# Optimization experiments

Measured on AMD Instinct MI355X. Metric: run time of the kernel, lower is better.

The kernel has to match this reference:

```python
import jax, jax.numpy as jnp
import numpy as np

B, S, C, H, FF = 2, 1500, 1024, 16, 4096
D = C // H  # head_dim = 64
EPS = 1e-5


def _ln(x, g, b):
    # LayerNorm over channel dim (axis=1) for (B, C, S) tensors
    mu = jnp.mean(x, axis=1, keepdims=True)
    var = jnp.mean(jnp.square(x - mu), axis=1, keepdims=True)
    return (x - mu) * jax.lax.rsqrt(var + EPS) * g[None, :, None] + b[None, :, None]


def setup_inputs() -> dict:
    key = jax.random.key(0)
    ks = jax.random.split(key, 24)
    w = lambda k, shp: (jax.random.normal(k, shp, dtype=jnp.float32) * 0.02)
    return {
        "hidden_states": jax.random.normal(ks[0], (B, C, 1, S), dtype=jnp.float32),
        "attention_mask": jnp.ones((B, S), dtype=jnp.float32),
        "position_bias": jax.random.normal(ks[1], (B, H, S, S), dtype=jnp.float32),
        "Wq": w(ks[2], (C, C)), "bq": jnp.zeros((C,), jnp.float32),
        "Wk": w(ks[3], (C, C)), "bk": jnp.zeros((C,), jnp.float32),
        "Wv": w(ks[4], (C, C)), "bv": jnp.zeros((C,), jnp.float32),
        "Wo": w(ks[5], (C, C)), "bo": jnp.zeros((C,), jnp.float32),
        "Wg": w(ks[6], (8, D)), "bg": jnp.zeros((8,), jnp.float32),
        "gru_const": jnp.ones((1, 1, H, 1), jnp.float32),
        "ln1_g": jnp.ones((C,), jnp.float32), "ln1_b": jnp.zeros((C,), jnp.float32),
        "W1": w(ks[7], (FF, C)), "b1": jnp.zeros((FF,), jnp.float32),
        "W2": w(ks[8], (C, FF)), "b2": jnp.zeros((C,), jnp.float32),
        "ln2_g": jnp.ones((C,), jnp.float32), "ln2_b": jnp.zeros((C,), jnp.float32),
    }


def reference(hidden_states, attention_mask, position_bias,
              Wq, bq, Wk, bk, Wv, bv, Wo, bo, Wg, bg, gru_const,
              ln1_g, ln1_b, W1, b1, W2, b2, ln2_g, ln2_b):
    x = hidden_states[:, :, 0, :]  # (B, C, S)

    # --- GRU-style relative-position gate ---
    xh = x.reshape(B, H, D, S)  # (B, H, D, S)
    # conv2d with (8, D, 1, 1) kernel on (B, D, H, S) == per-head linear D->8
    g8 = jnp.einsum('od,bhds->bohs', Wg, xh) + bg[None, :, None, None]  # (B, 8, H, S)
    gate_a = jax.nn.sigmoid(jnp.sum(g8[:, :4], axis=1, keepdims=True))  # (B, 1, H, S)
    gate_b = jax.nn.sigmoid(jnp.sum(g8[:, 4:], axis=1, keepdims=True))  # (B, 1, H, S)
    gate = gate_a * (gate_b * gru_const - 1.0) + 2.0  # (B, 1, H, S)
    qk_mask = gate[:, 0, :, :, None] * position_bias  # (B, H, Sq, Sk)

    # --- self-attention ---
    q = (jnp.einsum('oc,bcs->bos', Wq, x) + bq[None, :, None]).reshape(B, H, D, S)
    k = (jnp.einsum('oc,bcs->bos', Wk, x) + bk[None, :, None]).reshape(B, H, D, S)
    v = (jnp.einsum('oc,bcs->bos', Wv, x) + bv[None, :, None]).reshape(B, H, D, S)
    scale = 1.0 / jnp.sqrt(jnp.float32(D))
    kpm = (1.0 - attention_mask) * -10000.0  # (B, S)
    scores = jnp.einsum('bhdq,bhdk->bhqk', q, k) * scale + qk_mask + kpm[:, None, None, :]
    probs = jax.nn.softmax(scores, axis=-1)
    ctx = jnp.einsum('bhqk,bhdk->bhdq', probs, v).reshape(B, C, S)
    attn_out = jnp.einsum('oc,bcs->bos', Wo, ctx) + bo[None, :, None]

    h = _ln(x + attn_out, ln1_g, ln1_b)

    # --- FFN ---
    f = jax.nn.gelu(jnp.einsum('fc,bcs->bfs', W1, h) + b1[None, :, None], approximate=False)
    f = jnp.einsum('cf,bfs->bcs', W2, f) + b2[None, :, None]

    out = _ln(h + f, ln2_g, ln2_b)
    return out[:, :, None, :]  # (B, C, 1, S)
```

## Files before the change

kernel.cpp:

```cpp
#include <hip/hip_runtime.h>
#include <cstddef>
#include <cstdint>

#define Bn 2
#define Sn 1500
#define SPn 1536
#define Cn 1024
#define Hn 16
#define FFn 4096

typedef __attribute__((ext_vector_type(8))) short bf16x8;
typedef __attribute__((ext_vector_type(4))) float f32x4;
typedef unsigned short u16;
typedef unsigned int u32;

__device__ __forceinline__ u16 f2bu(float f) {
  unsigned u = __float_as_uint(f);
  return (u16)((u + 0x7fffu + ((u >> 16) & 1u)) >> 16);
}

__device__ __forceinline__ void gl_lds16(const u16* g, u16* l) {
  __builtin_amdgcn_global_load_lds(
      (__attribute__((address_space(1))) void*)(uintptr_t)g,
      (__attribute__((address_space(3))) void*)(u32)(uintptr_t)l,
      16, 0, 0);
}

__global__ __launch_bounds__(256) void k_pre(
    const float* __restrict__ x,
    const float* __restrict__ Wq, const float* __restrict__ Wk,
    const float* __restrict__ Wv, const float* __restrict__ Wo,
    const float* __restrict__ W1, const float* __restrict__ W2,
    const float* __restrict__ bq, const float* __restrict__ bk,
    const float* __restrict__ bv,
    const float* __restrict__ Wg, const float* __restrict__ bg,
    const float* __restrict__ gc,
    float* __restrict__ xT, u16* __restrict__ xTb,
    u16* __restrict__ wqkvb, u16* __restrict__ wob,
    u16* __restrict__ w1b, u16* __restrict__ w2b, float* __restrict__ bqkv,
    float* __restrict__ gate)
{
  const int bid = blockIdx.x;
  if (bid < 3072) {
    __shared__ float t[32][33];
    const int c0 = (bid & 31) * 32, s0 = ((bid >> 5) % 48) * 32, b = bid / 1536;
    const int tx = threadIdx.x & 31, ty = threadIdx.x >> 5;
#pragma unroll
    for (int i = 0; i < 32; i += 8) {
      int c = c0 + ty + i, s = s0 + tx;
      t[ty + i][tx] = (s < Sn) ? x[((size_t)b * Cn + c) * Sn + s] : 0.f;
    }
    __syncthreads();
#pragma unroll
    for (int i = 0; i < 32; i += 8) {
      int s = s0 + ty + i, c = c0 + tx;
      float v = t[tx][ty + i];
      size_t o = ((size_t)b * SPn + s) * Cn + c;
      xT[o] = v;
      xTb[o] = f2bu(v);
    }
    return;
  }
  if (bid < 15363) {
    int i = (bid - 3072) * 256 + threadIdx.x;
    const float* src;
    u16* dst;
    int j;
    if (i < 786432) {
      src = (i < 262144) ? Wq : ((i < 524288) ? Wk : Wv);
      j = i & 262143;
      dst = wqkvb + (size_t)i * 4;
    } else if (i < 1048576) {
      src = Wo; j = i - 786432; dst = wob + (size_t)j * 4;
    } else if (i < 2097152) {
      src = W1; j = i - 1048576; dst = w1b + (size_t)j * 4;
    } else if (i < 3145728) {
      src = W2; j = i - 2097152; dst = w2b + (size_t)j * 4;
    } else {
      int k = i - 3145728;
      const float* bsrc = (k < 256) ? bq : ((k < 512) ? bk : bv);
      float4 v = *(const float4*)(bsrc + (k & 255) * 4);
      *(float4*)(bqkv + k * 4) = v;
      return;
    }
    float4 v = *(const float4*)(src + (size_t)j * 4);
    ushort4 o;
    o.x = f2bu(v.x); o.y = f2bu(v.y); o.z = f2bu(v.z); o.w = f2bu(v.w);
    *(ushort4*)dst = o;
    return;
  }
  {
    const int gid = bid - 15363;
    const int b = gid / 96, h = (gid / 6) & 15;
    const int s = (gid % 6) * 256 + threadIdx.x;
    const bool vld = s < Sn;
    const float* xp = x + ((size_t)b * Cn + h * 64) * Sn + (vld ? s : 0);
    float dot[8];
#pragma unroll
    for (int o = 0; o < 8; o++) dot[o] = 0.f;
    for (int d = 0; d < 64; d++) {
      float v = xp[(size_t)d * Sn];
#pragma unroll
      for (int o = 0; o < 8; o++) dot[o] += Wg[o * 64 + d] * v;
    }
    float sa = dot[0] + dot[1] + dot[2] + dot[3] + bg[0] + bg[1] + bg[2] + bg[3];
    float sb = dot[4] + dot[5] + dot[6] + dot[7] + bg[4] + bg[5] + bg[6] + bg[7];
    float ga = 1.f / (1.f + __expf(-sa));
    float gb = 1.f / (1.f + __expf(-sb));
    float gv = ga * (gb * gc[h] - 1.f) + 2.f;
    gate[((size_t)b * Hn + h) * SPn + s] = vld ? gv : 0.f;
  }
}

__global__ __launch_bounds__(256) void k_transpose_out(
    const float* __restrict__ oT, float* __restrict__ o)
{
  __shared__ float t[32][33];
  const int b = blockIdx.z, c0 = blockIdx.x * 32, s0 = blockIdx.y * 32;
  const int tx = threadIdx.x & 31, ty = threadIdx.x >> 5;
#pragma unroll
  for (int i = 0; i < 32; i += 8) {
    int s = s0 + ty + i, c = c0 + tx;
    t[ty + i][tx] = oT[((size_t)b * SPn + s) * Cn + c];
  }
  __syncthreads();
#pragma unroll
  for (int i = 0; i < 32; i += 8) {
    int c = c0 + ty + i, s = s0 + tx;
    if (s < Sn) o[((size_t)b * Cn + c) * Sn + s] = t[tx][ty + i];
  }
}

template <int EPI, int SPLIT, int TM>
__global__ __launch_bounds__(256) void k_gemm(
    const u16* __restrict__ A, const u16* __restrict__ X,
    const float* __restrict__ bias, void* __restrict__ out, void* __restrict__ out2,
    u16* __restrict__ vT, int M, int Kst, int Ktot)
{
  constexpr int NI = TM / 32;
  const int zz = blockIdx.z;
  const int b = zz / SPLIT, half = zz % SPLIT;
  const int Kc = Ktot / SPLIT;
  const int m0 = blockIdx.x * TM;
  const int s0 = blockIdx.y * 128;
  const int tid = threadIdx.x;
  const int lane = tid & 63;
  const int wid = tid >> 6;
  const int wm = (wid >> 1) * (TM / 2);
  const int wn = (wid & 1) * 64;
  const int l15 = lane & 15;
  const int g4 = lane >> 4;

  __shared__ __align__(16) u16 lA[TM][64];
  __shared__ __align__(16) u16 lX[128][64];

  f32x4 acc[NI][4];
  f32x4 zr; zr[0] = 0.f; zr[1] = 0.f; zr[2] = 0.f; zr[3] = 0.f;
#pragma unroll
  for (int i = 0; i < NI; i++)
#pragma unroll
    for (int j = 0; j < 4; j++) acc[i][j] = zr;

  const int rlo = lane >> 3;
  const int cg = (lane & 7) ^ rlo;
  const int kbeg = half * Kc;
  const u16* gA = A + (size_t)(m0 + wid * (TM / 4) + rlo) * Kst + cg * 8 + kbeg;
  const u16* gX = X + ((size_t)b * SPn + s0 + wid * 32 + rlo) * Kst + cg * 8 + kbeg;
  u16* lAp = &lA[0][0] + wid * (TM / 4) * 64;
  u16* lXp = &lX[0][0] + wid * 2048;
  const size_t rstep8 = (size_t)8 * Kst;

  for (int kt = 0; kt < Kc; kt += 64) {
    __syncthreads();
#pragma unroll
    for (int j = 0; j < TM / 32; j++)
      gl_lds16(gA + j * rstep8 + kt, lAp + j * 512);
#pragma unroll
    for (int j = 0; j < 4; j++)
      gl_lds16(gX + j * rstep8 + kt, lXp + j * 512);
    __syncthreads();
#pragma unroll
    for (int ks = 0; ks < 2; ks++) {
      bf16x8 af[NI], bfr[4];
#pragma unroll
      for (int i = 0; i < NI; i++) {
        int ra = wm + i * 16 + l15;
        af[i] = *(const bf16x8*)&lA[ra][((ks * 4 + g4) ^ (ra & 7)) * 8];
      }
#pragma unroll
      for (int j = 0; j < 4; j++) {
        int rb = wn + j * 16 + l15;
        bfr[j] = *(const bf16x8*)&lX[rb][((ks * 4 + g4) ^ (rb & 7)) * 8];
      }
#pragma unroll
      for (int i = 0; i < NI; i++)
#pragma unroll
        for (int j = 0; j < 4; j++)
          acc[i][j] = __builtin_amdgcn_mfma_f32_16x16x32_bf16(af[i], bfr[j], acc[i][j], 0, 0, 0);
    }
  }

  const float hsc = (half == 0) ? 1.f : 0.f;
  void* outp = (half == 0) ? out : out2;
#pragma unroll
  for (int i = 0; i < NI; i++) {
    int o = m0 + wm + i * 16 + g4 * 4;
    float4 bs = *(const float4*)(bias + o);
#pragma unroll
    for (int j = 0; j < 4; j++) {
      int s = s0 + wn + j * 16 + l15;
      size_t oidx = ((size_t)b * SPn + s) * M + o;
      f32x4 v = acc[i][j];
      float x0 = v[0] + bs.x * hsc, x1 = v[1] + bs.y * hsc;
      float x2 = v[2] + bs.z * hsc, x3 = v[3] + bs.w * hsc;
      if (EPI == 0) {
        float4 st; st.x = x0; st.y = x1; st.z = x2; st.w = x3;
        *(float4*)((float*)outp + oidx) = st;
      } else if (EPI == 1) {
        x0 = 0.5f * x0 * (1.f + erff(x0 * 0.70710678118654752f));
        x1 = 0.5f * x1 * (1.f + erff(x1 * 0.70710678118654752f));
        x2 = 0.5f * x2 * (1.f + erff(x2 * 0.70710678118654752f));
        x3 = 0.5f * x3 * (1.f + erff(x3 * 0.70710678118654752f));
        ushort4 st;
        st.x = f2bu(x0); st.y = f2bu(x1); st.z = f2bu(x2); st.w = f2bu(x3);
        *(ushort4*)((u16*)outp + oidx) = st;
      } else {
        ushort4 st;
        st.x = f2bu(x0); st.y = f2bu(x1); st.z = f2bu(x2); st.w = f2bu(x3);
        *(ushort4*)((u16*)outp + oidx) = st;
        if (EPI == 2 && o >= 2048) {
          int oo = o - 2048;
          int h = oo >> 6, d = oo & 63;
          u16* vp = vT + ((size_t)(b * Hn + h) * 64 + d) * SPn + s;
          vp[0] = st.x;
          vp[SPn] = st.y;
          vp[2 * SPn] = st.z;
          vp[3 * SPn] = st.w;
        }
      }
    }
  }
}

__global__ __launch_bounds__(256) void k_flash_mfma(
    const u16* __restrict__ qkv,
    const u16* __restrict__ vT,
    const float* __restrict__ pb,
    const float* __restrict__ am,
    const float* __restrict__ gate,
    u16* __restrict__ ctx)
{
  const int bh = blockIdx.y, b = bh >> 4, h = bh & 15;
  const int q0 = blockIdx.x * 64;
  const int tid = threadIdx.x;
  const int lane = tid & 63, wid = tid >> 6;
  const int l15 = lane & 15, g4 = lane >> 4;
  const int q = q0 + wid * 16 + l15;

  __shared__ __align__(16) u16 kls[64][72];
  __shared__ __align__(16) u16 vls[64][72];
  __shared__ __align__(16) u16 pls[4][16][72];
  __shared__ float kpm[64];

  bf16x8 qf[2];
  {
    const u16* qp = qkv + ((size_t)b * SPn + q) * 3072 + h * 64 + g4 * 8;
    qf[0] = *(const bf16x8*)qp;
    qf[1] = *(const bf16x8*)(qp + 32);
  }
  const float gr = gate[(size_t)bh * SPn + q];
  const int qpb = (q < Sn) ? q : (Sn - 1);
  const float* pbrow = pb + ((size_t)bh * Sn + qpb) * Sn;

  float m = -3.0e38f, l = 0.f;
  f32x4 accO[4];
  f32x4 zr; zr[0] = 0.f; zr[1] = 0.f; zr[2] = 0.f; zr[3] = 0.f;
#pragma unroll
  for (int i = 0; i < 4; i++) accO[i] = zr;

  for (int kt = 0; kt < 24; kt++) {
    const int k0 = kt * 64;
    __syncthreads();
#pragma unroll
    for (int i = 0; i < 2; i++) {
      int idx = i * 256 + tid;
      int row = idx >> 3, c8 = (idx & 7) * 8;
      *(int4*)&kls[row][c8] =
          *(const int4*)(qkv + ((size_t)b * SPn + k0 + row) * 3072 + 1024 + h * 64 + c8);
      *(int4*)&vls[row][c8] =
          *(const int4*)(vT + ((size_t)bh * 64 + row) * SPn + k0 + c8);
    }
    if (tid < 64) {
      int sk = k0 + tid;
      kpm[tid] = (sk < Sn) ? (1.f - am[b * Sn + sk]) * -10000.f : -1e30f;
    }
    __syncthreads();

    f32x4 sAcc[4];
#pragma unroll
    for (int km = 0; km < 4; km++) {
      sAcc[km] = zr;
#pragma unroll
      for (int dc = 0; dc < 2; dc++) {
        bf16x8 af = *(const bf16x8*)&kls[km * 16 + l15][dc * 32 + g4 * 8];
        sAcc[km] = __builtin_amdgcn_mfma_f32_16x16x32_bf16(af, qf[dc], sAcc[km], 0, 0, 0);
      }
    }

    float sc[16];
    const bool tail = (k0 + 63 >= Sn);
#pragma unroll
    for (int km = 0; km < 4; km++) {
      int kk = k0 + km * 16 + g4 * 4;
      float4 pbv;
      if (!tail) {
        pbv = *(const float4*)(pbrow + kk);
      } else {
        pbv.x = (kk + 0 < Sn) ? pbrow[kk + 0] : 0.f;
        pbv.y = (kk + 1 < Sn) ? pbrow[kk + 1] : 0.f;
        pbv.z = (kk + 2 < Sn) ? pbrow[kk + 2] : 0.f;
        pbv.w = (kk + 3 < Sn) ? pbrow[kk + 3] : 0.f;
      }
      float4 kp = *(const float4*)&kpm[km * 16 + g4 * 4];
      sc[km * 4 + 0] = sAcc[km][0] * 0.125f + gr * pbv.x + kp.x;
      sc[km * 4 + 1] = sAcc[km][1] * 0.125f + gr * pbv.y + kp.y;
      sc[km * 4 + 2] = sAcc[km][2] * 0.125f + gr * pbv.z + kp.z;
      sc[km * 4 + 3] = sAcc[km][3] * 0.125f + gr * pbv.w + kp.w;
    }

    float mloc = sc[0];
#pragma unroll
    for (int i = 1; i < 16; i++) mloc = fmaxf(mloc, sc[i]);
    mloc = fmaxf(mloc, __shfl_xor(mloc, 16));
    mloc = fmaxf(mloc, __shfl_xor(mloc, 32));

    if (mloc > m + 8.f) {
      float corr = __expf(m - mloc);
      m = mloc;
      l *= corr;
#pragma unroll
      for (int i = 0; i < 4; i++) {
        accO[i][0] *= corr; accO[i][1] *= corr;
        accO[i][2] *= corr; accO[i][3] *= corr;
      }
    }

    float ls = 0.f;
#pragma unroll
    for (int i = 0; i < 16; i++) {
      float p = __expf(sc[i] - m);
      sc[i] = p;
      ls += p;
    }
    ls += __shfl_xor(ls, 16);
    ls += __shfl_xor(ls, 32);
    l += ls;

#pragma unroll
    for (int km = 0; km < 4; km++) {
      u32 lo = (u32)f2bu(sc[km * 4 + 0]) | ((u32)f2bu(sc[km * 4 + 1]) << 16);
      u32 hi = (u32)f2bu(sc[km * 4 + 2]) | ((u32)f2bu(sc[km * 4 + 3]) << 16);
      u32* dst = (u32*)&pls[wid][l15][km * 16 + g4 * 4];
      dst[0] = lo; dst[1] = hi;
    }

    bf16x8 pf[2];
    pf[0] = *(const bf16x8*)&pls[wid][l15][g4 * 8];
    pf[1] = *(const bf16x8*)&pls[wid][l15][32 + g4 * 8];
#pragma unroll
    for (int dm = 0; dm < 4; dm++) {
#pragma unroll
      for (int kc = 0; kc < 2; kc++) {
        bf16x8 af = *(const bf16x8*)&vls[dm * 16 + l15][kc * 32 + g4 * 8];
        accO[dm] = __builtin_amdgcn_mfma_f32_16x16x32_bf16(af, pf[kc], accO[dm], 0, 0, 0);
      }
    }
  }

  float inv = 1.f / l;
  const bool qv = q < Sn;
#pragma unroll
  for (int dm = 0; dm < 4; dm++) {
    ushort4 st;
    st.x = f2bu(qv ? accO[dm][0] * inv : 0.f);
    st.y = f2bu(qv ? accO[dm][1] * inv : 0.f);
    st.z = f2bu(qv ? accO[dm][2] * inv : 0.f);
    st.w = f2bu(qv ? accO[dm][3] * inv : 0.f);
    *(ushort4*)(ctx + ((size_t)b * SPn + q) * Cn + h * 64 + dm * 16 + g4 * 4) = st;
  }
}

__global__ __launch_bounds__(256) void k_ln3(
    const float* __restrict__ r1, const float* __restrict__ r2,
    const float* __restrict__ r3,
    const float* __restrict__ g, const float* __restrict__ be,
    float* __restrict__ outF, u16* __restrict__ outB)
{
  const int s = blockIdx.x, b = blockIdx.y;
  const size_t base = ((size_t)b * SPn + s) * Cn;
  __shared__ float buf[Cn];
  __shared__ float red[8];
  const int tid = threadIdx.x;
  float sum = 0.f;
#pragma unroll
  for (int i = 0; i < 4; i++) {
    int c = tid + i * 256;
    float t = r1[base + c] + r2[base + c] + r3[base + c];
    buf[c] = t;
    sum += t;
  }
#pragma unroll
  for (int mk = 1; mk < 64; mk <<= 1) sum += __shfl_xor(sum, mk);
  if ((tid & 63) == 0) red[tid >> 6] = sum;
  __syncthreads();
  float mu = (red[0] + red[1] + red[2] + red[3]) * (1.f / Cn);
  float vs = 0.f;
#pragma unroll
  for (int i = 0; i < 4; i++) {
    int c = tid + i * 256;
    float d = buf[c] - mu;
    vs += d * d;
  }
#pragma unroll
  for (int mk = 1; mk < 64; mk <<= 1) vs += __shfl_xor(vs, mk);
  if ((tid & 63) == 0) red[4 + (tid >> 6)] = vs;
  __syncthreads();
  float var = (red[4] + red[5] + red[6] + red[7]) * (1.f / Cn);
  float rstd = rsqrtf(var + 1e-5f);
#pragma unroll
  for (int i = 0; i < 4; i++) {
    int c = tid + i * 256;
    float val = (buf[c] - mu) * rstd * g[c] + be[c];
    outF[base + c] = val;
    if (outB) outB[base + c] = f2bu(val);
  }
}

extern "C" void kernel_launch(void* const* d_in, const int* in_sizes, int n_in,
                              void* d_out, int out_size, void* d_ws, size_t ws_size,
                              hipStream_t stream)
{
  const float* x    = (const float*)d_in[0];
  const float* am   = (const float*)d_in[1];
  const float* pb   = (const float*)d_in[2];
  const float* Wq   = (const float*)d_in[3];
  const float* bq   = (const float*)d_in[4];
  const float* Wk   = (const float*)d_in[5];
  const float* bk   = (const float*)d_in[6];
  const float* Wv   = (const float*)d_in[7];
  const float* bv   = (const float*)d_in[8];
  const float* Wo   = (const float*)d_in[9];
  const float* bo   = (const float*)d_in[10];
  const float* Wg   = (const float*)d_in[11];
  const float* bg   = (const float*)d_in[12];
  const float* gc   = (const float*)d_in[13];
  const float* ln1g = (const float*)d_in[14];
  const float* ln1b = (const float*)d_in[15];
  const float* W1   = (const float*)d_in[16];
  const float* b1   = (const float*)d_in[17];
  const float* W2   = (const float*)d_in[18];
  const float* b2   = (const float*)d_in[19];
  const float* ln2g = (const float*)d_in[20];
  const float* ln2b = (const float*)d_in[21];

  char* ws = (char*)d_ws;
  float* xT     = (float*)(ws + 0);
  u16*   xTb    = (u16*)(ws + 12582912);
  u16*   wqkvb  = (u16*)(ws + 18874368);
  u16*   wob    = (u16*)(ws + 25165824);
  u16*   w1b    = (u16*)(ws + 27262976);
  u16*   w2b    = (u16*)(ws + 35651584);
  float* bqkv   = (float*)(ws + 44040192);
  float* gate   = (float*)(ws + 44052480);
  u16*   qkvB   = (u16*)(ws + 44249088);
  u16*   vT     = (u16*)(ws + 63123456);
  float* attnTa = (float*)(ws + 69414912);
  float* attnTb = (float*)(ws + 81997824);
  u16*   ctxT   = xTb;
  float* hT     = (float*)(ws + 44249088);
  u16*   hTb    = wqkvb;
  u16*   fT     = (u16*)(ws + 56832000);
  float* f2Ta   = (float*)(ws + 0);
  float* f2Tb   = (float*)(ws + 81997824);
  float* outT   = (float*)(ws + 12582912);

  dim3 blk(256);
  k_pre<<<dim3(15555), blk, 0, stream>>>(x, Wq, Wk, Wv, Wo, W1, W2, bq, bk, bv,
                                         Wg, bg, gc, xT, xTb, wqkvb, wob, w1b,
                                         w2b, bqkv, gate);

  k_gemm<2, 1, 96><<<dim3(32, 12, Bn), blk, 0, stream>>>(
      wqkvb, xTb, bqkv, qkvB, qkvB, vT, 3072, 1024, 1024);
  k_flash_mfma<<<dim3(SPn / 64, Bn * Hn), blk, 0, stream>>>(qkvB, vT, pb, am, gate, ctxT);
  k_gemm<0, 2, 64><<<dim3(16, 12, Bn * 2), blk, 0, stream>>>(
      wob, ctxT, bo, attnTa, attnTb, (u16*)nullptr, 1024, 1024, 1024);
  k_ln3<<<dim3(SPn, Bn), blk, 0, stream>>>(xT, attnTa, attnTb, ln1g, ln1b, hT, hTb);
  k_gemm<1, 1, 128><<<dim3(32, 12, Bn), blk, 0, stream>>>(
      w1b, hTb, b1, fT, fT, (u16*)nullptr, 4096, 1024, 1024);
  k_gemm<0, 2, 64><<<dim3(16, 12, Bn * 2), blk, 0, stream>>>(
      w2b, fT, b2, f2Ta, f2Tb, (u16*)nullptr, 1024, 4096, 4096);
  k_ln3<<<dim3(SPn, Bn), blk, 0, stream>>>(hT, f2Ta, f2Tb, ln2g, ln2b, outT, (u16*)nullptr);
  k_transpose_out<<<dim3(Cn / 32, SPn / 32, Bn), blk, 0, stream>>>(outT, (float*)d_out);
}
```

Measured before the change: 295.5 us.

## Prefetch K/V tiles in flash attention and store split-K partials in bf16

The flash-attention kernel now loads the next K/V tile into registers while the current tile is computed, and writes it to LDS after a barrier. It also precomputes the full key padding mask into shared memory once per block, and issues the position-bias loads early. The Wo and W2 split-K GEMMs now write their partial sums as bf16 instead of fp32, and the LayerNorm kernel reads these with vectorised float4/ushort4 loads and keeps values in registers rather than a shared buffer. This cuts memory traffic and hides load latency, at the cost of extra rounding in the residual partial sums and more registers and LDS in the attention kernel.

```diff
diff --git a/kernel.cpp b/kernel.cpp
--- a/kernel.cpp
+++ b/kernel.cpp
@@ -17,6 +17,9 @@
 __device__ __forceinline__ u16 f2bu(float f) {
   unsigned u = __float_as_uint(f);
   return (u16)((u + 0x7fffu + ((u >> 16) & 1u)) >> 16);
+}
+__device__ __forceinline__ float bu2f(u16 v) {
+  return __uint_as_float(((u32)v) << 16);
 }
 
 __device__ __forceinline__ void gl_lds16(const u16* g, u16* l) {
@@ -228,7 +231,7 @@
         ushort4 st;
         st.x = f2bu(x0); st.y = f2bu(x1); st.z = f2bu(x2); st.w = f2bu(x3);
         *(ushort4*)((u16*)outp + oidx) = st;
-        if (EPI == 2 && o >= 2048) {
+        if (vT != nullptr && o >= 2048) {
           int oo = o - 2048;
           int h = oo >> 6, d = oo & 63;
           u16* vp = vT + ((size_t)(b * Hn + h) * 64 + d) * SPn + s;
@@ -260,7 +263,14 @@
   __shared__ __align__(16) u16 kls[64][72];
   __shared__ __align__(16) u16 vls[64][72];
   __shared__ __align__(16) u16 pls[4][16][72];
-  __shared__ float kpm[64];
+  __shared__ float kpm[SPn];
+
+  const int r0 = tid >> 3, c80 = (tid & 7) * 8;
+  const int r1 = (256 + tid) >> 3, c81 = c80;
+  const u16* kg0 = qkv + ((size_t)b * SPn + r0) * 3072 + 1024 + h * 64 + c80;
+  const u16* kg1 = qkv + ((size_t)b * SPn + r1) * 3072 + 1024 + h * 64 + c81;
+  const u16* vg0 = vT + ((size_t)bh * 64 + r0) * SPn + c80;
+  const u16* vg1 = vT + ((size_t)bh * 64 + r1) * SPn + c81;
 
   bf16x8 qf[2];
   {
@@ -272,6 +282,23 @@
   const int qpb = (q < Sn) ? q : (Sn - 1);
   const float* pbrow = pb + ((size_t)bh * Sn + qpb) * Sn;
 
+  {
+    int4 k0v = *(const int4*)kg0;
+    int4 k1v = *(const int4*)kg1;
+    int4 v0v = *(const int4*)vg0;
+    int4 v1v = *(const int4*)vg1;
+#pragma unroll
+    for (int j = 0; j < 6; j++) {
+      int idx = tid + j * 256;
+      kpm[idx] = (idx < Sn) ? (1.f - am[b * Sn + idx]) * -10000.f : -1e30f;
+    }
+    *(int4*)&kls[r0][c80] = k0v;
+    *(int4*)&kls[r1][c81] = k1v;
+    *(int4*)&vls[r0][c80] = v0v;
+    *(int4*)&vls[r1][c81] = v1v;
+  }
+  __syncthreads();
+
   float m = -3.0e38f, l = 0.f;
   f32x4 accO[4];
   f32x4 zr; zr[0] = 0.f; zr[1] = 0.f; zr[2] = 0.f; zr[3] = 0.f;
@@ -280,21 +307,29 @@
 
   for (int kt = 0; kt < 24; kt++) {
     const int k0 = kt * 64;
-    __syncthreads();
-#pragma unroll
-    for (int i = 0; i < 2; i++) {
-      int idx = i * 256 + tid;
-      int row = idx >> 3, c8 = (idx & 7) * 8;
-      *(int4*)&kls[row][c8] =
-          *(const int4*)(qkv + ((size_t)b * SPn + k0 + row) * 3072 + 1024 + h * 64 + c8);
-      *(int4*)&vls[row][c8] =
-          *(const int4*)(vT + ((size_t)bh * 64 + row) * SPn + k0 + c8);
-    }
-    if (tid < 64) {
-      int sk = k0 + tid;
-      kpm[tid] = (sk < Sn) ? (1.f - am[b * Sn + sk]) * -10000.f : -1e30f;
-    }
-    __syncthreads();
+    int4 krn0, krn1, vrn0, vrn1;
+    if (kt < 23) {
+      const int k0n = k0 + 64;
+      krn0 = *(const int4*)(kg0 + (size_t)k0n * 3072);
+      krn1 = *(const int4*)(kg1 + (size_t)k0n * 3072);
+      vrn0 = *(const int4*)(vg0 + k0n);
+      vrn1 = *(const int4*)(vg1 + k0n);
+    }
+    float4 pbv[4];
+    if (kt < 23) {
+#pragma unroll
+      for (int km = 0; km < 4; km++)
+        pbv[km] = *(const float4*)(pbrow + k0 + km * 16 + g4 * 4);
+    } else {
+#pragma unroll
+      for (int km = 0; km < 4; km++) {
+        int kk = k0 + km * 16 + g4 * 4;
+        pbv[km].x = (kk + 0 < Sn) ? pbrow[kk + 0] : 0.f;
+        pbv[km].y = (kk + 1 < Sn) ? pbrow[kk + 1] : 0.f;
+        pbv[km].z = (kk + 2 < Sn) ? pbrow[kk + 2] : 0.f;
+        pbv[km].w = (kk + 3 < Sn) ? pbrow[kk + 3] : 0.f;
+      }
+    }
 
     f32x4 sAcc[4];
 #pragma unroll
@@ -308,24 +343,14 @@
     }
 
     float sc[16];
-    const bool tail = (k0 + 63 >= Sn);
 #pragma unroll
     for (int km = 0; km < 4; km++) {
       int kk = k0 + km * 16 + g4 * 4;
-      float4 pbv;
-      if (!tail) {
-        pbv = *(const float4*)(pbrow + kk);
-      } else {
-        pbv.x = (kk + 0 < Sn) ? pbrow[kk + 0] : 0.f;
-        pbv.y = (kk + 1 < Sn) ? pbrow[kk + 1] : 0.f;
-        pbv.z = (kk + 2 < Sn) ? pbrow[kk + 2] : 0.f;
-        pbv.w = (kk + 3 < Sn) ? pbrow[kk + 3] : 0.f;
-      }
-      float4 kp = *(const float4*)&kpm[km * 16 + g4 * 4];
-      sc[km * 4 + 0] = sAcc[km][0] * 0.125f + gr * pbv.x + kp.x;
-      sc[km * 4 + 1] = sAcc[km][1] * 0.125f + gr * pbv.y + kp.y;
-      sc[km * 4 + 2] = sAcc[km][2] * 0.125f + gr * pbv.z + kp.z;
-      sc[km * 4 + 3] = sAcc[km][3] * 0.125f + gr * pbv.w + kp.w;
+      float4 kp = *(const float4*)&kpm[kk];
+      sc[km * 4 + 0] = sAcc[km][0] * 0.125f + gr * pbv[km].x + kp.x;
+      sc[km * 4 + 1] = sAcc[km][1] * 0.125f + gr * pbv[km].y + kp.y;
+      sc[km * 4 + 2] = sAcc[km][2] * 0.125f + gr * pbv[km].z + kp.z;
+      sc[km * 4 + 3] = sAcc[km][3] * 0.125f + gr * pbv[km].w + kp.w;
     }
 
     float mloc = sc[0];
@@ -374,6 +399,15 @@
         bf16x8 af = *(const bf16x8*)&vls[dm * 16 + l15][kc * 32 + g4 * 8];
         accO[dm] = __builtin_amdgcn_mfma_f32_16x16x32_bf16(af, pf[kc], accO[dm], 0, 0, 0);
       }
+    }
+
+    __syncthreads();
+    if (kt < 23) {
+      *(int4*)&kls[r0][c80] = krn0;
+      *(int4*)&kls[r1][c81] = krn1;
+      *(int4*)&vls[r0][c80] = vrn0;
+      *(int4*)&vls[r1][c81] = vrn1;
+      __syncthreads();
     }
   }
 
@@ -391,48 +425,49 @@
 }
 
 __global__ __launch_bounds__(256) void k_ln3(
-    const float* __restrict__ r1, const float* __restrict__ r2,
-    const float* __restrict__ r3,
+    const float* __restrict__ r1, const u16* __restrict__ r2,
+    const u16* __restrict__ r3,
     const float* __restrict__ g, const float* __restrict__ be,
     float* __restrict__ outF, u16* __restrict__ outB)
 {
   const int s = blockIdx.x, b = blockIdx.y;
   const size_t base = ((size_t)b * SPn + s) * Cn;
-  __shared__ float buf[Cn];
   __shared__ float red[8];
   const int tid = threadIdx.x;
-  float sum = 0.f;
-#pragma unroll
-  for (int i = 0; i < 4; i++) {
-    int c = tid + i * 256;
-    float t = r1[base + c] + r2[base + c] + r3[base + c];
-    buf[c] = t;
-    sum += t;
-  }
+  const int c = tid * 4;
+  float4 a = *(const float4*)(r1 + base + c);
+  ushort4 v2 = *(const ushort4*)(r2 + base + c);
+  ushort4 v3 = *(const ushort4*)(r3 + base + c);
+  float t0 = a.x + bu2f(v2.x) + bu2f(v3.x);
+  float t1 = a.y + bu2f(v2.y) + bu2f(v3.y);
+  float t2 = a.z + bu2f(v2.z) + bu2f(v3.z);
+  float t3 = a.w + bu2f(v2.w) + bu2f(v3.w);
+  float sum = t0 + t1 + t2 + t3;
 #pragma unroll
   for (int mk = 1; mk < 64; mk <<= 1) sum += __shfl_xor(sum, mk);
   if ((tid & 63) == 0) red[tid >> 6] = sum;
   __syncthreads();
   float mu = (red[0] + red[1] + red[2] + red[3]) * (1.f / Cn);
-  float vs = 0.f;
-#pragma unroll
-  for (int i = 0; i < 4; i++) {
-    int c = tid + i * 256;
-    float d = buf[c] - mu;
-    vs += d * d;
-  }
+  float d0 = t0 - mu, d1 = t1 - mu, d2 = t2 - mu, d3 = t3 - mu;
+  float vs = d0 * d0 + d1 * d1 + d2 * d2 + d3 * d3;
 #pragma unroll
   for (int mk = 1; mk < 64; mk <<= 1) vs += __shfl_xor(vs, mk);
   if ((tid & 63) == 0) red[4 + (tid >> 6)] = vs;
   __syncthreads();
   float var = (red[4] + red[5] + red[6] + red[7]) * (1.f / Cn);
   float rstd = rsqrtf(var + 1e-5f);
-#pragma unroll
-  for (int i = 0; i < 4; i++) {
-    int c = tid + i * 256;
-    float val = (buf[c] - mu) * rstd * g[c] + be[c];
-    outF[base + c] = val;
-    if (outB) outB[base + c] = f2bu(val);
+  float4 gv = *(const float4*)(g + c);
+  float4 bv = *(const float4*)(be + c);
+  float o0 = d0 * rstd * gv.x + bv.x;
+  float o1 = d1 * rstd * gv.y + bv.y;
+  float o2 = d2 * rstd * gv.z + bv.z;
+  float o3 = d3 * rstd * gv.w + bv.w;
+  float4 st; st.x = o0; st.y = o1; st.z = o2; st.w = o3;
+  *(float4*)(outF + base + c) = st;
+  if (outB) {
+    ushort4 sb;
+    sb.x = f2bu(o0); sb.y = f2bu(o1); sb.z = f2bu(o2); sb.w = f2bu(o3);
+    *(ushort4*)(outB + base + c) = sb;
   }
 }
 
@@ -474,14 +509,14 @@
   float* gate   = (float*)(ws + 44052480);
   u16*   qkvB   = (u16*)(ws + 44249088);
   u16*   vT     = (u16*)(ws + 63123456);
-  float* attnTa = (float*)(ws + 69414912);
-  float* attnTb = (float*)(ws + 81997824);
+  u16*   attnTa = (u16*)(ws + 69414912);
+  u16*   attnTb = (u16*)(ws + 81997824);
   u16*   ctxT   = xTb;
   float* hT     = (float*)(ws + 44249088);
   u16*   hTb    = wqkvb;
   u16*   fT     = (u16*)(ws + 56832000);
-  float* f2Ta   = (float*)(ws + 0);
-  float* f2Tb   = (float*)(ws + 81997824);
+  u16*   f2Ta   = (u16*)(ws + 0);
+  u16*   f2Tb   = (u16*)(ws + 81997824);
   float* outT   = (float*)(ws + 12582912);
 
   dim3 blk(256);
@@ -492,12 +527,12 @@
   k_gemm<2, 1, 96><<<dim3(32, 12, Bn), blk, 0, stream>>>(
       wqkvb, xTb, bqkv, qkvB, qkvB, vT, 3072, 1024, 1024);
   k_flash_mfma<<<dim3(SPn / 64, Bn * Hn), blk, 0, stream>>>(qkvB, vT, pb, am, gate, ctxT);
-  k_gemm<0, 2, 64><<<dim3(16, 12, Bn * 2), blk, 0, stream>>>(
+  k_gemm<2, 2, 64><<<dim3(16, 12, Bn * 2), blk, 0, stream>>>(
       wob, ctxT, bo, attnTa, attnTb, (u16*)nullptr, 1024, 1024, 1024);
   k_ln3<<<dim3(SPn, Bn), blk, 0, stream>>>(xT, attnTa, attnTb, ln1g, ln1b, hT, hTb);
   k_gemm<1, 1, 128><<<dim3(32, 12, Bn), blk, 0, stream>>>(
       w1b, hTb, b1, fT, fT, (u16*)nullptr, 4096, 1024, 1024);
-  k_gemm<0, 2, 64><<<dim3(16, 12, Bn * 2), blk, 0, stream>>>(
+  k_gemm<2, 2, 64><<<dim3(16, 12, Bn * 2), blk, 0, stream>>>(
       w2b, fT, b2, f2Ta, f2Tb, (u16*)nullptr, 1024, 4096, 4096);
   k_ln3<<<dim3(SPn, Bn), blk, 0, stream>>>(hT, f2Ta, f2Tb, ln2g, ln2b, outT, (u16*)nullptr);
   k_transpose_out<<<dim3(Cn / 32, SPn / 32, Bn), blk, 0, stream>>>(outT, (float*)d_out);
```

Result: faster. 267.6 us (-9.4%).
